# Performance work log

Measured on AMD Instinct MI355X. Metric: run time of the kernel, lower is better.

## Reference

```python
import jax, jax.numpy as jnp
import numpy as np

# ---- static config (matches init_kwargs) ----
D = 1152      # hidden_size
I = 4608      # mlp intermediate = 4*D
DEPTH = 2     # transformer blocks
SA_DEPTH = 3  # spatial adapter depth
P_LAT = 2     # latent patch size
OUT_C = 8     # in_channels*2 (learn_sigma)
FREQ = 256    # timestep frequency embedding size
NV = 4        # num_views
B = 2         # true batch (BN = B*NV = 8)
LAT = 32      # latent H=W
COND = 512    # conditioning image H=W

# ---- BitNet b1.58 / HGRN primitives ----

def rmsnorm(x, eps=1e-8):
    return x * jax.lax.rsqrt(jnp.mean(jnp.square(x), axis=-1, keepdims=True) + eps)

def layernorm(x, gamma=None, beta=None, eps=1e-6):
    mu = jnp.mean(x, axis=-1, keepdims=True)
    xc = x - mu
    y = xc * jax.lax.rsqrt(jnp.mean(jnp.square(xc), axis=-1, keepdims=True) + eps)
    if gamma is not None:
        y = y * gamma + beta
    return y

def _act_quant(x):  # per-token int8 absmax quantization
    s = 127.0 / jnp.clip(jnp.max(jnp.abs(x), axis=-1, keepdims=True), 1e-5, None)
    return jnp.clip(jnp.round(x * s), -128.0, 127.0) / s

def _w_quant(w):    # ternary (1.58-bit) weight quantization, global absmean scale
    s = 1.0 / jnp.clip(jnp.mean(jnp.abs(w)), 1e-5, None)
    return jnp.clip(jnp.round(w * s), -1.0, 1.0) / s

def _ste(x, q):     # straight-through estimator
    return x + jax.lax.stop_gradient(q - x)

def bitlinear(x, w, b=None):
    # FusedBitLinear: RMSNorm -> int8 act quant -> ternary weight matmul
    xn = rmsnorm(x)
    y = _ste(xn, _act_quant(xn)) @ _ste(w, _w_quant(w)).T
    return y if b is None else y + b

def conv2d(x, w, b, stride):
    y = jax.lax.conv_general_dilated(x, w, (stride, stride), 'VALID',
                                     dimension_numbers=('NCHW', 'OIHW', 'NCHW'))
    return y + b[None, :, None, None]

def hgrn_attn(x, wi, wf, wg, wo):
    # HGRN gated-linear attention: h_t = f_t*h_{t-1} + silu(i_t)*(1-f_t),
    # output RMSNorm-swish-gated then o-projected. Element-wise recurrence.
    f = jax.nn.sigmoid(bitlinear(x, wf))
    v = jax.nn.silu(bitlinear(x, wi)) * (1.0 - f)
    g = bitlinear(x, wg)
    def step(h, fv):
        ft, vt = fv
        h = ft * h + vt
        return h, h
    _, o = jax.lax.scan(step, jnp.zeros_like(v[:, 0]),
                        (jnp.swapaxes(f, 0, 1), jnp.swapaxes(v, 0, 1)))
    o = jnp.swapaxes(o, 0, 1)
    o = rmsnorm(o) * g * jax.nn.sigmoid(g)
    return bitlinear(o, wo)

def hgrn_mlp(x, w_gate, w_down):
    gate, y = jnp.split(bitlinear(x, w_gate), 2, axis=-1)
    return bitlinear(jax.nn.silu(gate) * y, w_down)

def modulate(x, shift, scale):
    return x * (1.0 + scale[:, None]) + shift[:, None]

# ---- full adapter forward ----

def _forward(x, t, y, x_cond, ref_tokens, num_views, P):
    BN = x.shape[0]
    # conditioning vector c = TimestepEmbedder(t) + prompt_proj(y)
    half = FREQ // 2
    freqs = jnp.exp(-np.log(10000.0) * jnp.arange(half, dtype=jnp.float32) / half)
    ang = t[:, None] * freqs[None]
    t_emb = jnp.concatenate([jnp.cos(ang), jnp.sin(ang)], axis=-1)
    t_emb = bitlinear(jax.nn.silu(bitlinear(t_emb, P['te_w1'], P['te_b1'])), P['te_w2'], P['te_b2'])
    c = t_emb + bitlinear(y, P['pp_w'], P['pp_b'])

    h = conv2d(x_cond, P['sa_pe_w'], P['sa_pe_b'], 16)      # [BN, D, 32, 32]
    Hc = h.shape[-1]
    h = h.reshape(BN, D, Hc * Hc).transpose(0, 2, 1)
    feats = []
    for i in range(SA_DEPTH):
        h = hgrn_mlp(layernorm(h, P['sa_ln_g'][i], P['sa_ln_b'][i], eps=1e-5),
                     P['sa_gate_w'][i], P['sa_down_w'][i])
        h = h.transpose(0, 2, 1).reshape(BN, D, Hc, Hc)
        h = conv2d(h, P['sa_dc_w'][i], P['sa_dc_b'][i], 2)
        Hc //= 2
        h = h.reshape(BN, D, Hc * Hc).transpose(0, 2, 1)
        feats.append(h)

    # patchify latents + pos embed + spatial cond feature (grid-matched)
    xt = conv2d(x, P['xe_w'], P['xe_b'], P_LAT)             # [BN, D, 16, 16]
    Hp = xt.shape[-1]
    xt = xt.reshape(BN, D, Hp * Hp).transpose(0, 2, 1) + P['pos_embed'] + feats[0]
    L = xt.shape[1]
    b = BN // num_views
    ref_rep = jnp.repeat(ref_tokens, num_views, axis=0)     # repeat_interleave dim 0

    for l in range(DEPTH):
        mod = bitlinear(jax.nn.silu(c), P['blk_ada_w'][l], P['blk_ada_b'][l])
        sh_a, sc_a, g_a, sh_m, sc_m, g_m = jnp.split(mod, 6, axis=-1)
        xm = modulate(layernorm(xt), sh_a, sc_a)
        self_out = hgrn_attn(xm, P['blk_sa_wi'][l], P['blk_sa_wf'][l], P['blk_sa_wg'][l], P['blk_sa_wo'][l])
        # multi-view attention: sequence axis = views
        mv_in = xm.reshape(b, num_views, L, D).transpose(0, 2, 1, 3).reshape(b * L, num_views, D)
        mv_out = hgrn_attn(mv_in, P['blk_mv_wi'][l], P['blk_mv_wf'][l], P['blk_mv_wg'][l], P['blk_mv_wo'][l])
        mv_out = mv_out.reshape(b, L, num_views, D).transpose(0, 2, 1, 3).reshape(BN, L, D)
        ref_out = hgrn_attn(ref_rep, P['blk_rf_wi'][l], P['blk_rf_wf'][l], P['blk_rf_wg'][l], P['blk_rf_wo'][l])
        xt = xt + g_a[:, None] * (self_out + mv_out + ref_out)
        xm = modulate(layernorm(xt), sh_m, sc_m)
        xt = xt + g_m[:, None] * hgrn_mlp(xm, P['blk_gate_w'][l], P['blk_down_w'][l])

    # final layer + unpatchify
    mod = bitlinear(jax.nn.silu(c), P['fl_ada_w'], P['fl_ada_b'])
    shift, scale = jnp.split(mod, 2, axis=-1)
    xt = bitlinear(modulate(layernorm(xt), shift, scale), P['fl_w'], P['fl_b'])
    xt = xt.reshape(BN, Hp, Hp, P_LAT, P_LAT, OUT_C).transpose(0, 5, 1, 3, 2, 4)
    return xt.reshape(BN, OUT_C, Hp * P_LAT, Hp * P_LAT)

PARAM_SHAPES = {
    'xe_w': (D, 4, P_LAT, P_LAT), 'xe_b': (D,), 'pos_embed': (1, 256, D),
    'te_w1': (D, FREQ), 'te_b1': (D,), 'te_w2': (D, D), 'te_b2': (D,),
    'pp_w': (D, 768), 'pp_b': (D,),
    'sa_pe_w': (D, 6, 16, 16), 'sa_pe_b': (D,),
    'sa_ln_g': (SA_DEPTH, D), 'sa_ln_b': (SA_DEPTH, D),
    'sa_gate_w': (SA_DEPTH, 2 * I, D), 'sa_down_w': (SA_DEPTH, D, I),
    'sa_dc_w': (SA_DEPTH, D, D, 2, 2), 'sa_dc_b': (SA_DEPTH, D),
    'blk_ada_w': (DEPTH, 6 * D, D), 'blk_ada_b': (DEPTH, 6 * D),
    'blk_sa_wi': (DEPTH, D, D), 'blk_sa_wf': (DEPTH, D, D), 'blk_sa_wg': (DEPTH, D, D), 'blk_sa_wo': (DEPTH, D, D),
    'blk_mv_wi': (DEPTH, D, D), 'blk_mv_wf': (DEPTH, D, D), 'blk_mv_wg': (DEPTH, D, D), 'blk_mv_wo': (DEPTH, D, D),
    'blk_rf_wi': (DEPTH, D, D), 'blk_rf_wf': (DEPTH, D, D), 'blk_rf_wg': (DEPTH, D, D), 'blk_rf_wo': (DEPTH, D, D),
    'blk_gate_w': (DEPTH, 2 * I, D), 'blk_down_w': (DEPTH, D, I),
    'fl_w': (P_LAT * P_LAT * OUT_C, D), 'fl_b': (P_LAT * P_LAT * OUT_C,),
    'fl_ada_w': (2 * D, D), 'fl_ada_b': (2 * D,),
}
_ZEROS = {'xe_b', 'te_b1', 'te_b2', 'pp_b', 'sa_pe_b', 'sa_ln_b', 'sa_dc_b',
          'blk_ada_b', 'fl_b', 'fl_ada_b'}
_ONES = {'sa_ln_g'}

def setup_inputs() -> dict:
    key = jax.random.key(0)
    ks = iter(jax.random.split(key, 8 + len(PARAM_SHAPES)))
    inp = {
        'x': jax.random.normal(next(ks), (B * NV, 4, LAT, LAT), jnp.float32),
        't': jax.random.uniform(next(ks), (B * NV,), jnp.float32, 0.0, 1000.0),
        'y': jax.random.normal(next(ks), (B * NV, 768), jnp.float32),
        'x_cond': jax.random.normal(next(ks), (B * NV, 6, COND, COND), jnp.float32),
        'ref_tokens': jax.random.normal(next(ks), (B, 256, D), jnp.float32),
        'num_views': NV,
    }
    for name, shp in PARAM_SHAPES.items():
        if name in _ZEROS:
            inp[name] = jnp.zeros(shp, jnp.float32)
        elif name in _ONES:
            inp[name] = jnp.ones(shp, jnp.float32)
        else:
            inp[name] = 0.02 * jax.random.normal(next(ks), shp, jnp.float32)
    return inp

def reference(x, t, y, x_cond, ref_tokens, num_views,
              xe_w, xe_b, pos_embed, te_w1, te_b1, te_w2, te_b2, pp_w, pp_b,
              sa_pe_w, sa_pe_b, sa_ln_g, sa_ln_b, sa_gate_w, sa_down_w, sa_dc_w, sa_dc_b,
              blk_ada_w, blk_ada_b,
              blk_sa_wi, blk_sa_wf, blk_sa_wg, blk_sa_wo,
              blk_mv_wi, blk_mv_wf, blk_mv_wg, blk_mv_wo,
              blk_rf_wi, blk_rf_wf, blk_rf_wg, blk_rf_wo,
              blk_gate_w, blk_down_w, fl_w, fl_b, fl_ada_w, fl_ada_b):
    P = dict(xe_w=xe_w, xe_b=xe_b, pos_embed=pos_embed, te_w1=te_w1, te_b1=te_b1,
             te_w2=te_w2, te_b2=te_b2, pp_w=pp_w, pp_b=pp_b, sa_pe_w=sa_pe_w,
             sa_pe_b=sa_pe_b, sa_ln_g=sa_ln_g, sa_ln_b=sa_ln_b, sa_gate_w=sa_gate_w,
             sa_down_w=sa_down_w, sa_dc_w=sa_dc_w, sa_dc_b=sa_dc_b, blk_ada_w=blk_ada_w,
             blk_ada_b=blk_ada_b, blk_sa_wi=blk_sa_wi, blk_sa_wf=blk_sa_wf,
             blk_sa_wg=blk_sa_wg, blk_sa_wo=blk_sa_wo, blk_mv_wi=blk_mv_wi,
             blk_mv_wf=blk_mv_wf, blk_mv_wg=blk_mv_wg, blk_mv_wo=blk_mv_wo,
             blk_rf_wi=blk_rf_wi, blk_rf_wf=blk_rf_wf, blk_rf_wg=blk_rf_wg,
             blk_rf_wo=blk_rf_wo, blk_gate_w=blk_gate_w, blk_down_w=blk_down_w,
             fl_w=fl_w, fl_b=fl_b, fl_ada_w=fl_ada_w, fl_ada_b=fl_ada_b)
    return _forward(x, t, y, x_cond, ref_tokens, int(num_views), P)
```

## Files before the change

kernel.cpp:

```cpp
#include <hip/hip_runtime.h>

#define DEV __device__ __forceinline__

typedef __attribute__((ext_vector_type(4))) int i32x4;
typedef __attribute__((ext_vector_type(4))) double f64x4;


struct WList { const float* p[37]; long long n[37]; };
struct WOffs { long long o[37]; };

DEV int2 xcd_swz(int gridx)
{
    const int nwg = (int)gridDim.x, b = (int)blockIdx.x;
    const int q = nwg >> 3, r = nwg & 7, xcd = b & 7, idx = b >> 3;
    const int lb = (xcd < r ? xcd*(q+1) : r*(q+1) + (xcd-r)*q) + idx;
    return make_int2(lb % gridx, lb / gridx);
}

__global__ void k_mfma64_probe(double* __restrict__ out)
{
    const int lane = threadIdx.x;
    double a = (double)(1 + lane);
    double b = (double)(101 + 3*lane);
    f64x4 acc = {0.0, 0.0, 0.0, 0.0};
    acc = __builtin_amdgcn_mfma_f64_16x16x4f64(a, b, acc, 0, 0, 0);
#pragma unroll
    for (int r = 0; r < 4; ++r) out[lane*4 + r] = acc[r];
}

__global__ void k_mfma64_check(const double* __restrict__ probe, int* __restrict__ flag)
{
    if (threadIdx.x != 0) return;
    int best = 0;
    for (int c = 0; c < 16 && !best; ++c) {
        const int a_alt = c & 1, b_alt = (c >> 1) & 1, dv = (c >> 2) & 3;
        double Amat[16][4], Bmat[4][16];
        for (int l = 0; l < 64; ++l) {
            int ai = a_alt ? (l >> 2) : (l & 15);
            int ak = a_alt ? (l & 3)  : (l >> 4);
            Amat[ai][ak] = (double)(1 + l);
            int bj = b_alt ? (l >> 2) : (l & 15);
            int bk = b_alt ? (l & 3)  : (l >> 4);
            Bmat[bk][bj] = (double)(101 + 3*l);
        }
        double C[16][16];
        for (int i = 0; i < 16; ++i)
            for (int j = 0; j < 16; ++j) {
                double s = 0.0;
                for (int k = 0; k < 4; ++k) s += Amat[i][k] * Bmat[k][j];
                C[i][j] = s;
            }
        bool ok = true;
        for (int l = 0; l < 64 && ok; ++l)
            for (int r = 0; r < 4 && ok; ++r) {
                int ir = (dv & 2) ? (4*r + (l >> 4)) : (4*(l >> 4) + r);
                int ic = l & 15;
                if (dv & 1) { int t = ir; ir = ic; ic = t; }
                if (probe[l*4 + r] != C[ir][ic]) ok = false;
            }
        if (ok) best = 1 + c;
    }
    *flag = best;
}

__global__ void k_abssum_all(WList wl, double* __restrict__ partials)
{
    const int slot = blockIdx.y;
    const float* w = wl.p[slot];
    const long long n = wl.n[slot];
    __shared__ double sm[256];
    double s = 0.0;
    for (long long i = (long long)blockIdx.x*256 + threadIdx.x; i < n; i += 32LL*256)
        s += (double)fabsf(w[i]);
    sm[threadIdx.x] = s;
    __syncthreads();
    for (int k = 128; k > 0; k >>= 1) {
        if ((int)threadIdx.x < k) sm[threadIdx.x] += sm[threadIdx.x + k];
        __syncthreads();
    }
    if (threadIdx.x == 0) partials[slot*32 + blockIdx.x] = sm[0];
}

__global__ void k_abssum_fin(const double* __restrict__ partials, double* __restrict__ out)
{
    const int slot = blockIdx.x;
    if (threadIdx.x == 0) {
        double s = 0.0;
        for (int i = 0; i < 32; ++i) s += partials[slot*32 + i];
        out[slot] = s;
    }
}

__global__ void k_ternarize(WList wl, WOffs wo, const double* __restrict__ scales,
                            signed char* __restrict__ W8)
{
    const int slot = blockIdx.y;
    const float* w = wl.p[slot];
    const long long n4 = wl.n[slot] >> 2;
    const double dqw = fmax(scales[slot] / (double)wl.n[slot], 1e-5);
    const double thr = 0.5 * dqw;
    signed char* o = W8 + wo.o[slot];
    for (long long i = (long long)blockIdx.x*256 + threadIdx.x; i < n4; i += 64LL*256) {
        float4 v = *reinterpret_cast<const float4*>(w + i*4);
        float we[4] = {v.x, v.y, v.z, v.w};
        char r[4];
#pragma unroll
        for (int e = 0; e < 4; ++e) {
            double wd = (double)we[e];
            r[e] = (char)((wd > thr) - (wd < -thr));
        }
        *reinterpret_cast<char4*>(o + i*4) = make_char4(r[0], r[1], r[2], r[3]);
    }
}

__global__ void k_temb(const float* __restrict__ t, double* __restrict__ out)
{
    int b = blockIdx.x, j = threadIdx.x;
    double fr  = exp(-9.210340371976184 * (double)j / 128.0);
    double ang = (double)t[b] * fr;
    out[b*256 + j]       = cos(ang);
    out[b*256 + 128 + j] = sin(ang);
}

template<typename TI>
__global__ void k_rsq8(const TI* __restrict__ x, signed char* __restrict__ q8,
                       double* __restrict__ dscale, int K, int pre_silu)
{
    __shared__ double red[256], red2[256];
    const int row = blockIdx.x, tid = threadIdx.x;
    const TI* xr = x + (size_t)row*K;
    double ss = 0.0, am = 0.0;
    for (int i = tid; i < K; i += 256) {
        double v = (double)xr[i];
        if (pre_silu) v = v / (1.0 + exp(-v));
        ss += v*v; am = fmax(am, fabs(v));
    }
    red[tid] = ss; red2[tid] = am;
    __syncthreads();
    for (int s = 128; s > 0; s >>= 1) {
        if (tid < s) { red[tid] += red[tid+s]; red2[tid] = fmax(red2[tid], red2[tid+s]); }
        __syncthreads();
    }
    double rms = 1.0 / sqrt(red[0]/(double)K + 1e-8);
    double s   = 127.0 / fmax(red2[0]*rms, 1e-5);
    signed char* orow = q8 + (size_t)row*K;
    for (int i = tid; i < K; i += 256) {
        double v = (double)xr[i];
        if (pre_silu) v = v / (1.0 + exp(-v));
        orow[i] = (signed char)(int)fmin(fmax(rint(v*rms*s), -128.0), 127.0);
    }
    if (tid == 0) dscale[row] = s;
}

__global__ void k_lnq8(const double* __restrict__ x, signed char* __restrict__ q8,
                       double* __restrict__ dscale, int K,
                       const float* __restrict__ gamma, const float* __restrict__ beta,
                       const double* __restrict__ sh, const double* __restrict__ sc,
                       int modstride, double eps)
{
    extern __shared__ double rb[];
    __shared__ double red[256], red2[256];
    const int row = blockIdx.x, tid = threadIdx.x;
    const double* xr = x + (size_t)row*K;
    double s1 = 0.0;
    for (int i = tid; i < K; i += 256) { double v = xr[i]; rb[i] = v; s1 += v; }
    red[tid] = s1; __syncthreads();
    for (int s = 128; s > 0; s >>= 1) { if (tid < s) red[tid] += red[tid+s]; __syncthreads(); }
    double mu = red[0]/(double)K;
    __syncthreads();
    double s2 = 0.0;
    for (int i = tid; i < K; i += 256) { double d = rb[i]-mu; s2 += d*d; }
    red[tid] = s2; __syncthreads();
    for (int s = 128; s > 0; s >>= 1) { if (tid < s) red[tid] += red[tid+s]; __syncthreads(); }
    double r = 1.0 / sqrt(red[0]/(double)K + eps);
    const int bn = row >> 8;
    __syncthreads();
    double ss = 0.0, am = 0.0;
    for (int i = tid; i < K; i += 256) {
        double y = (rb[i]-mu)*r;
        if (gamma) y = y*(double)gamma[i] + (double)beta[i];
        if (sh)    y = y*(1.0 + sc[(size_t)bn*modstride + i]) + sh[(size_t)bn*modstride + i];
        rb[i] = y; ss += y*y; am = fmax(am, fabs(y));
    }
    red[tid] = ss; red2[tid] = am;
    __syncthreads();
    for (int s = 128; s > 0; s >>= 1) {
        if (tid < s) { red[tid] += red[tid+s]; red2[tid] = fmax(red2[tid], red2[tid+s]); }
        __syncthreads();
    }
    double rms = 1.0 / sqrt(red[0]/(double)K + 1e-8);
    double s   = 127.0 / fmax(red2[0]*rms, 1e-5);
    signed char* orow = q8 + (size_t)row*K;
    for (int i = tid; i < K; i += 256)
        orow[i] = (signed char)(int)fmin(fmax(rint(rb[i]*rms*s), -128.0), 127.0);
    if (tid == 0) dscale[row] = s;
}

__global__ void k_ogateq8(const double* __restrict__ O, const double* __restrict__ G,
                          signed char* __restrict__ q8, double* __restrict__ dscale, int K)
{
    extern __shared__ double rb[];
    __shared__ double red[256], red2[256];
    const int row = blockIdx.x, tid = threadIdx.x;
    const double* orow = O + (size_t)row*K;
    const double* grow = G + (size_t)row*K;
    double ss = 0.0;
    for (int i = tid; i < K; i += 256) { double v = orow[i]; rb[i] = v; ss += v*v; }
    red[tid] = ss; __syncthreads();
    for (int s = 128; s > 0; s >>= 1) { if (tid < s) red[tid] += red[tid+s]; __syncthreads(); }
    double rmso = 1.0 / sqrt(red[0]/(double)K + 1e-8);
    __syncthreads();
    double ss2 = 0.0, am = 0.0;
    for (int i = tid; i < K; i += 256) {
        double g = grow[i];
        double y = rb[i]*rmso * g / (1.0 + exp(-g));
        rb[i] = y; ss2 += y*y; am = fmax(am, fabs(y));
    }
    red[tid] = ss2; red2[tid] = am;
    __syncthreads();
    for (int s = 128; s > 0; s >>= 1) {
        if (tid < s) { red[tid] += red[tid+s]; red2[tid] = fmax(red2[tid], red2[tid+s]); }
        __syncthreads();
    }
    double rms = 1.0 / sqrt(red[0]/(double)K + 1e-8);
    double s   = 127.0 / fmax(red2[0]*rms, 1e-5);
    signed char* qrow = q8 + (size_t)row*K;
    for (int i = tid; i < K; i += 256)
        qrow[i] = (signed char)(int)fmin(fmax(rint(rb[i]*rms*s), -128.0), 127.0);
    if (tid == 0) dscale[row] = s;
}

__global__ void k_gatepre(double* __restrict__ F, double* __restrict__ I, long long n)
{
    long long i = (long long)blockIdx.x*256 + threadIdx.x;
    if (i >= n) return;
    double fp = F[i], ip = I[i];
    double f = 1.0/(1.0+exp(-fp));
    double v = (ip/(1.0+exp(-ip)))*(1.0-f);
    F[i] = f; I[i] = v;
}

__global__ void k_scan2(const double* __restrict__ F, const double* __restrict__ V,
                        double* __restrict__ O, int n_outer, long long outer_stride,
                        int n_inner, long long t_stride, int T)
{
    long long chain = (long long)blockIdx.x*blockDim.x + threadIdx.x;
    if (chain >= (long long)n_outer*n_inner) return;
    long long base = (chain / n_inner)*outer_stride + (chain % n_inner);
    double h = 0.0;
    for (int t = 0; t < T; ++t) {
        long long idx = base + (long long)t*t_stride;
        h = F[idx]*h + V[idx];
        O[idx] = h;
    }
}

__global__ void k_add(const double* __restrict__ a, const double* __restrict__ b,
                      double* __restrict__ o, int n)
{
    int i = blockIdx.x*256 + threadIdx.x;
    if (i < n) o[i] = a[i] + b[i];
}

__global__ void k_resid_attn(double* __restrict__ xt, const double* __restrict__ acc,
                             const double* __restrict__ refo, const double* __restrict__ mod)
{
    int idx = blockIdx.x*256 + threadIdx.x;
    int r = idx / 1152, d = idx - r*1152;
    int bn = r >> 8, l = r & 255;
    double ga = mod[(size_t)bn*6912 + 2*1152 + d];
    double rv = refo[((size_t)((bn>>2)*256 + l))*1152 + d];
    xt[idx] += ga*(acc[idx] + rv);
}

__global__ void k_resid_mlp(double* __restrict__ xt, const double* __restrict__ t2,
                            const double* __restrict__ mod)
{
    int idx = blockIdx.x*256 + threadIdx.x;
    int r = idx / 1152, d = idx - r*1152;
    int bn = r >> 8;
    xt[idx] += mod[(size_t)bn*6912 + 5*1152 + d] * t2[idx];
}

__global__ void k_patchify(const float* __restrict__ x, const float* __restrict__ w,
                           const float* __restrict__ bias, const float* __restrict__ pos,
                           const double* __restrict__ f0, double* __restrict__ xt)
{
    int idx = blockIdx.x*256 + threadIdx.x;
    int r = idx / 1152, o = idx - r*1152;
    int bn = r >> 8, p = r & 255;
    int y = p >> 4, xx = p & 15;
    double acc = (double)bias[o] + (double)pos[(size_t)p*1152 + o] + f0[idx];
#pragma unroll
    for (int c = 0; c < 4; ++c)
#pragma unroll
        for (int ky = 0; ky < 2; ++ky)
#pragma unroll
            for (int kx = 0; kx < 2; ++kx)
                acc += (double)x[((size_t)(bn*4 + c)*32 + 2*y+ky)*32 + 2*xx+kx]
                     * (double)w[o*16 + c*4 + ky*2 + kx];
    xt[idx] = acc;
}

__global__ void k_unpatch(const double* __restrict__ flo, float* __restrict__ out)
{
    int idx = blockIdx.x*256 + threadIdx.x;
    int xx = idx & 31, y = (idx>>5)&31, ch = (idx>>10)&7, b = idx>>13;
    int hp = y>>1, py = y&1, wp = xx>>1, px = xx&1;
    out[idx] = (float)flo[((size_t)(b*256 + hp*16 + wp))*32 + (py*2+px)*8 + ch];
}

template<int AMODE>
DEV void load_a4d(const void* __restrict__ A, int row, int k, int M, double o[4])
{
    if (row >= M) { o[0]=o[1]=o[2]=o[3]=0.0; return; }
    if constexpr (AMODE == 1) {
        const float* Af = (const float*)A;
        int b = row>>10, p = row&1023, oy = p>>5, ox = p&31;
        int c = k>>8, ky = (k>>4)&15, kx = k&15;
        float4 v = *reinterpret_cast<const float4*>(
            Af + (((size_t)(b*6+c)*512 + (size_t)(oy*16+ky))*512 + (size_t)(ox*16+kx)));
        o[0]=v.x; o[1]=v.y; o[2]=v.z; o[3]=v.w;
    } else {
        const double* Ad = (const double*)A;
        int b = row>>8, y = (row>>4)&15, x = row&15;
        int q = k/1152, c = k - q*1152, ky = q>>1, kx = q&1;
        const double* p = Ad + (size_t)(b*1024 + (2*y+ky)*32 + 2*x+kx)*1152 + c;
        o[0]=p[0]; o[1]=p[1]; o[2]=p[2]; o[3]=p[3];
    }
}

template<int WMODE>
DEV void load_w4d(const float* __restrict__ W, int row, int k, int Nb, int K, double o[4])
{
    if (row >= Nb) { o[0]=o[1]=o[2]=o[3]=0.0; return; }
    if constexpr (WMODE == 0) {
        float4 v = *reinterpret_cast<const float4*>(W + (size_t)row*K + k);
        o[0]=v.x; o[1]=v.y; o[2]=v.z; o[3]=v.w;
    } else {
        int q = k/1152, c = k - q*1152;
        const float* p = W + (size_t)row*4608 + (size_t)c*4 + q;
        o[0]=p[0]; o[1]=p[4]; o[2]=p[8]; o[3]=p[12];
    }
}

template<int AMODE, int WMODE>
__global__ __launch_bounds__(256)
void k_dgemm(const void* __restrict__ A, const float* __restrict__ W,
             const float* __restrict__ bias, double* __restrict__ C,
             int M, int N, int K, int gridx, const int* __restrict__ mfma_flag)
{
    __shared__ double As[64][17];
    __shared__ double Ws[64][17];
    const int tid = threadIdx.x;
    const int2 bxy = xcd_swz(gridx);
    const int m0 = bxy.y*64, n0 = bxy.x*64;
    const int lr = tid >> 2;
    const int lc = (tid & 3) * 4;
    const int flag = *mfma_flag;

    if (flag) {
        const int cmb = flag - 1;
        const int a_alt = cmb & 1, b_alt = (cmb >> 1) & 1, dv = (cmb >> 2) & 3;
        const int lane = tid & 63, wid = tid >> 6;
        const int wm = wid >> 1, wn = wid & 1;
        const int ai = a_alt ? (lane >> 2) : (lane & 15);
        const int ak = a_alt ? (lane & 3)  : (lane >> 4);
        const int bj = b_alt ? (lane >> 2) : (lane & 15);
        const int bk = b_alt ? (lane & 3)  : (lane >> 4);
        f64x4 fa[2][2];
#pragma unroll
        for (int i = 0; i < 2; ++i)
#pragma unroll
            for (int j = 0; j < 2; ++j) fa[i][j] = f64x4{0.0,0.0,0.0,0.0};

        for (int kt = 0; kt < K; kt += 16) {
            {
                double v[4];
                load_a4d<AMODE>(A, m0+lr, kt+lc, M, v);
                As[lr][lc+0]=v[0]; As[lr][lc+1]=v[1]; As[lr][lc+2]=v[2]; As[lr][lc+3]=v[3];
            }
            {
                double wv[4];
                load_w4d<WMODE>(W, n0+lr, kt+lc, N, K, wv);
                Ws[lr][lc+0]=wv[0]; Ws[lr][lc+1]=wv[1]; Ws[lr][lc+2]=wv[2]; Ws[lr][lc+3]=wv[3];
            }
            __syncthreads();
#pragma unroll
            for (int k4 = 0; k4 < 4; ++k4) {
                double a0 = As[wm*32 + ai][k4*4 + ak];
                double a1 = As[wm*32 + 16 + ai][k4*4 + ak];
                double b0 = Ws[wn*32 + bj][k4*4 + bk];
                double b1 = Ws[wn*32 + 16 + bj][k4*4 + bk];
                fa[0][0] = __builtin_amdgcn_mfma_f64_16x16x4f64(a0, b0, fa[0][0], 0, 0, 0);
                fa[0][1] = __builtin_amdgcn_mfma_f64_16x16x4f64(a0, b1, fa[0][1], 0, 0, 0);
                fa[1][0] = __builtin_amdgcn_mfma_f64_16x16x4f64(a1, b0, fa[1][0], 0, 0, 0);
                fa[1][1] = __builtin_amdgcn_mfma_f64_16x16x4f64(a1, b1, fa[1][1], 0, 0, 0);
            }
            __syncthreads();
        }
#pragma unroll
        for (int i = 0; i < 2; ++i)
#pragma unroll
            for (int j = 0; j < 2; ++j)
#pragma unroll
                for (int r = 0; r < 4; ++r) {
                    int ir = (dv & 2) ? (4*r + (lane >> 4)) : (4*(lane >> 4) + r);
                    int ic = lane & 15;
                    if (dv & 1) { int t = ir; ir = ic; ic = t; }
                    int row = m0 + wm*32 + i*16 + ir;
                    int col = n0 + wn*32 + j*16 + ic;
                    if (row < M && col < N)
                        C[(size_t)row*N + col] = fa[i][j][r] + (bias ? (double)bias[col] : 0.0);
                }
        return;
    }

    const int tx = tid & 15, ty = tid >> 4;
    double acc[4][4] = {};
    for (int kt = 0; kt < K; kt += 16) {
        {
            double v[4];
            load_a4d<AMODE>(A, m0+lr, kt+lc, M, v);
            As[lr][lc+0]=v[0]; As[lr][lc+1]=v[1]; As[lr][lc+2]=v[2]; As[lr][lc+3]=v[3];
        }
        {
            double wv[4];
            load_w4d<WMODE>(W, n0+lr, kt+lc, N, K, wv);
            Ws[lr][lc+0]=wv[0]; Ws[lr][lc+1]=wv[1]; Ws[lr][lc+2]=wv[2]; Ws[lr][lc+3]=wv[3];
        }
        __syncthreads();
#pragma unroll
        for (int k = 0; k < 16; ++k) {
            double a[4], b[4];
#pragma unroll
            for (int e = 0; e < 4; ++e) { a[e] = As[ty + 16*e][k]; b[e] = Ws[tx + 16*e][k]; }
#pragma unroll
            for (int i = 0; i < 4; ++i)
#pragma unroll
                for (int j = 0; j < 4; ++j) acc[i][j] += a[i]*b[j];
        }
        __syncthreads();
    }
#pragma unroll
    for (int i = 0; i < 4; ++i) {
        int row = m0 + ty + 16*i;
        if (row >= M) continue;
#pragma unroll
        for (int j = 0; j < 4; ++j) {
            int col = n0 + tx + 16*j;
            if (col >= N) continue;
            C[(size_t)row*N + col] = acc[i][j] + (bias ? (double)bias[col] : 0.0);
        }
    }
}

template<int GATE, int PRE>
__global__ __launch_bounds__(256)
void k_qgemm(const signed char* __restrict__ A8, const double* __restrict__ ascale,
             const float* __restrict__ Wf, const signed char* __restrict__ W8,
             const double* __restrict__ wsum, long long wcount,
             const float* __restrict__ bias, double* __restrict__ C,
             int M, int N, int K, int accum, int gridM)
{
    __shared__ __align__(16) signed char Als[4][128][16];
    __shared__ __align__(16) signed char Bls[4][128][16];
    __shared__ __align__(16) signed char B2ls[GATE?4:1][GATE?128:1][16];
    const int tid = threadIdx.x;
    const int lane = tid & 63, wid = tid >> 6;
    const int wr = wid >> 1, wc = wid & 1;
    const int2 bxy = xcd_swz(gridM);
    const int m0 = bxy.x*128, n0 = bxy.y*128;
    const int ks = lane >> 4, fr = lane & 15;

    const double dqw = fmax(*wsum / (double)wcount, 1e-5);
    const double thr = 0.5 * dqw;

    i32x4 acc[4][4];
    i32x4 acc2[GATE?4:1][4];
#pragma unroll
    for (int i = 0; i < 4; ++i)
#pragma unroll
        for (int j = 0; j < 4; ++j) {
            acc[i][j] = i32x4{0,0,0,0};
            if constexpr (GATE) acc2[i][j] = i32x4{0,0,0,0};
        }

    for (int kt = 0; kt < K; kt += 64) {
#pragma unroll
        for (int c = 0; c < 2; ++c) {
            int idx = tid + c*256;
            int row = idx & 127, kslot = idx >> 7;
            i32x4 v = {0,0,0,0};
            if (m0 + row < M)
                v = *reinterpret_cast<const i32x4*>(A8 + (size_t)(m0+row)*K + kt + kslot*16);
            *reinterpret_cast<i32x4*>(&Als[kslot][row][0]) = v;
        }
#pragma unroll
        for (int c = 0; c < 2; ++c) {
            int idx = tid + c*256;
            int row = idx & 127, kslot = idx >> 7;
            i32x4 pv = {0,0,0,0};
            if (n0 + row < N) {
                if constexpr (PRE) {
                    pv = *reinterpret_cast<const i32x4*>(W8 + (size_t)(n0+row)*K + kt + kslot*16);
                } else {
                    const float* wp = Wf + (size_t)(n0+row)*K + kt + kslot*16;
#pragma unroll
                    for (int d = 0; d < 4; ++d) {
                        float4 wv = *reinterpret_cast<const float4*>(wp + d*4);
                        float we[4] = {wv.x, wv.y, wv.z, wv.w};
                        unsigned p = 0;
#pragma unroll
                        for (int e = 0; e < 4; ++e) {
                            double wd = (double)we[e];
                            int q = (wd > thr) - (wd < -thr);
                            p |= ((unsigned)(q & 255)) << (8*e);
                        }
                        pv[d] = (int)p;
                    }
                }
            }
            *reinterpret_cast<i32x4*>(&Bls[kslot][row][0]) = pv;
        }
        if constexpr (GATE) {
#pragma unroll
            for (int c = 0; c < 2; ++c) {
                int idx = tid + c*256;
                int row = idx & 127, kslot = idx >> 7;
                i32x4 pv = {0,0,0,0};
                if (n0 + row < N) {
                    if constexpr (PRE) {
                        pv = *reinterpret_cast<const i32x4*>(W8 + (size_t)(n0+row+N)*K + kt + kslot*16);
                    } else {
                        const float* wp = Wf + (size_t)(n0+row+N)*K + kt + kslot*16;
#pragma unroll
                        for (int d = 0; d < 4; ++d) {
                            float4 wv = *reinterpret_cast<const float4*>(wp + d*4);
                            float we[4] = {wv.x, wv.y, wv.z, wv.w};
                            unsigned p = 0;
#pragma unroll
                            for (int e = 0; e < 4; ++e) {
                                double wd = (double)we[e];
                                int q = (wd > thr) - (wd < -thr);
                                p |= ((unsigned)(q & 255)) << (8*e);
                            }
                            pv[d] = (int)p;
                        }
                    }
                }
                *reinterpret_cast<i32x4*>(&B2ls[kslot][row][0]) = pv;
            }
        }
        __syncthreads();
        i32x4 a[4];
#pragma unroll
        for (int i = 0; i < 4; ++i)
            a[i] = *reinterpret_cast<const i32x4*>(&Als[ks][wr*64 + i*16 + fr][0]);
#pragma unroll
        for (int j = 0; j < 4; ++j) {
            i32x4 b = *reinterpret_cast<const i32x4*>(&Bls[ks][wc*64 + j*16 + fr][0]);
#pragma unroll
            for (int i = 0; i < 4; ++i)
                acc[i][j] = __builtin_amdgcn_mfma_i32_16x16x64_i8(a[i], b, acc[i][j], 0, 0, 0);
            if constexpr (GATE) {
                i32x4 b2 = *reinterpret_cast<const i32x4*>(&B2ls[ks][wc*64 + j*16 + fr][0]);
#pragma unroll
                for (int i = 0; i < 4; ++i)
                    acc2[i][j] = __builtin_amdgcn_mfma_i32_16x16x64_i8(a[i], b2, acc2[i][j], 0, 0, 0);
            }
        }
        __syncthreads();
    }

#pragma unroll
    for (int i = 0; i < 4; ++i) {
#pragma unroll
        for (int r = 0; r < 4; ++r) {
            int row = m0 + wr*64 + i*16 + (lane>>4)*4 + r;
            if (row >= M) continue;
            double mul = dqw / ascale[row];
#pragma unroll
            for (int j = 0; j < 4; ++j) {
                int col = n0 + wc*64 + j*16 + (lane & 15);
                if (col >= N) continue;
                size_t o = (size_t)row*N + col;
                if constexpr (GATE) {
                    double g = (double)acc[i][j][r] * mul;
                    double y = (double)acc2[i][j][r] * mul;
                    C[o] = g/(1.0+exp(-g)) * y;
                } else {
                    double v = (double)acc[i][j][r] * mul;
                    if (bias) v += (double)bias[col];
                    C[o] = accum ? C[o] + v : v;
                }
            }
        }
    }
}

extern "C" void kernel_launch(void* const* d_in, const int* in_sizes, int n_in,
                              void* d_out, int out_size, void* d_ws, size_t ws_size,
                              hipStream_t stream)
{
    (void)in_sizes; (void)n_in; (void)out_size;
    auto in = [&](int i){ return (const float*)d_in[i]; };

    const float *X = in(0), *T = in(1), *Y = in(2), *XC = in(3), *REF = in(4);
    const float *xe_w = in(6), *xe_b = in(7), *pos = in(8);
    const float *te_w1 = in(9), *te_b1 = in(10), *te_w2 = in(11), *te_b2 = in(12);
    const float *pp_w = in(13), *pp_b = in(14);
    const float *sa_pe_w = in(15), *sa_pe_b = in(16);
    const float *sa_ln_g = in(17), *sa_ln_b = in(18);
    const float *sa_gate_w = in(19), *sa_down_w = in(20);
    const float *sa_dc_w = in(21), *sa_dc_b = in(22);
    const float *ada_w = in(23), *ada_b = in(24);
    const float *sa_wi = in(25), *sa_wf = in(26), *sa_wg = in(27), *sa_wo = in(28);
    const float *mv_wi = in(29), *mv_wf = in(30), *mv_wg = in(31), *mv_wo = in(32);
    const float *rf_wi = in(33), *rf_wf = in(34), *rf_wg = in(35), *rf_wo = in(36);
    const float *gate_w = in(37), *down_w = in(38);
    const float *fl_w = in(39), *fl_b = in(40), *fl_ada_w = in(41), *fl_ada_b = in(42);
    float* OUT = (float*)d_out;

    size_t off = 0;
    auto AL = [&](size_t bytes){ off = (off+255)&~(size_t)255; size_t r = off; off += bytes; return r; };
    const size_t oScale = AL(37*8);
    const size_t oPart  = AL(37*32*8);
    const size_t oProbe = AL(64*4*8);
    const size_t oFlag  = AL(256);
    const size_t oSM1 = AL(8*1152*8), oSM2 = AL(8*1152*8), oSM3 = AL(8*1152*8);
    const size_t oCB  = AL(8*1152*8);
    const size_t oMOD = AL(8*6912*8);
    const size_t oH   = AL((size_t)8192*1152*8);
    const size_t oINT = AL((size_t)1024*4608*8);
    const size_t oF0  = AL((size_t)2048*1152*8);
    const size_t oXT  = AL((size_t)2048*1152*8);
    const size_t oFB  = AL((size_t)2048*1152*8);
    const size_t oIB  = AL((size_t)2048*1152*8);
    const size_t oGB  = AL((size_t)2048*1152*8);
    const size_t oRO  = AL((size_t)512*1152*8);
    const size_t oQ8X = AL((size_t)2048*1152);
    const size_t oQ8I = AL((size_t)1024*4608);
    const size_t oQ8O = AL((size_t)2048*1152);
    const size_t oQ8R = AL((size_t)512*1152);
    const size_t oQ8T = AL((size_t)8*1152);
    const size_t oQ8C = AL((size_t)8*1152);
    const size_t oDSX = AL(2048*8), oDSI = AL(1024*8), oDSO = AL(2048*8);
    const size_t oDSR = AL(512*8),  oDST = AL(8*8),    oDSC = AL(8*8);
    if (off > ws_size) return;

    WList wl{}; WOffs wo{};
    long long wn[37];
    int nw = 0;
    auto addw = [&](const float* w, long long n){ wl.p[nw]=w; wl.n[nw]=n; wn[nw]=n; nw++; };
    addw(te_w1, 294912); addw(te_w2, 1327104); addw(pp_w, 884736);
    addw(sa_gate_w, 10616832); addw(sa_down_w, 5308416);
    for (int l = 0; l < 2; ++l) {
        addw(ada_w + (size_t)l*7962624, 7962624);
        addw(sa_wi + (size_t)l*1327104, 1327104);
        addw(sa_wf + (size_t)l*1327104, 1327104);
        addw(sa_wg + (size_t)l*1327104, 1327104);
        addw(sa_wo + (size_t)l*1327104, 1327104);
        addw(mv_wi + (size_t)l*1327104, 1327104);
        addw(mv_wf + (size_t)l*1327104, 1327104);
        addw(mv_wg + (size_t)l*1327104, 1327104);
        addw(mv_wo + (size_t)l*1327104, 1327104);
        addw(rf_wi + (size_t)l*1327104, 1327104);
        addw(rf_wf + (size_t)l*1327104, 1327104);
        addw(rf_wg + (size_t)l*1327104, 1327104);
        addw(rf_wo + (size_t)l*1327104, 1327104);
        addw(gate_w + (size_t)l*10616832, 10616832);
        addw(down_w + (size_t)l*5308416, 5308416);
    }
    addw(fl_ada_w, 2654208); addw(fl_w, 36864);

    size_t off_saved = off;
    long long wtot = 0;
    for (int i = 0; i < 37; ++i) { wo.o[i] = wtot; wtot += (wn[i] + 255) & ~255LL; }
    const size_t oW8 = AL((size_t)wtot);
    const bool useW8 = (off <= ws_size);
    if (!useW8) off = off_saved;

    int schunk = 1024;
    size_t oINTb = 0, oQ8Ib = 0, oQ8Xb = 0, oDSXb = 0, oDSIb = 0;
    if (useW8) {
        size_t off_w8 = off;
        oINTb = AL((size_t)4096*4608*8); oQ8Ib = AL((size_t)4096*4608);
        oQ8Xb = AL((size_t)4096*1152);   oDSXb = AL(4096*8); oDSIb = AL(4096*8);
        if (off <= ws_size) schunk = 4096;
        else {
            off = off_w8;
            oINTb = AL((size_t)2048*4608*8); oQ8Ib = AL((size_t)2048*4608); oDSIb = AL(2048*8);
            if (off <= ws_size) schunk = 2048;
            else off = off_w8;
        }
    }

    char* w8p = (char*)d_ws;
    double* scales = (double*)(w8p + oScale);
    double* parts  = (double*)(w8p + oPart);
    double* probeD = (double*)(w8p + oProbe);
    int*    mflag  = (int*)(w8p + oFlag);
    double *SM1=(double*)(w8p+oSM1), *SM2=(double*)(w8p+oSM2), *SM3=(double*)(w8p+oSM3);
    double *CB=(double*)(w8p+oCB), *MOD=(double*)(w8p+oMOD);
    double *H=(double*)(w8p+oH), *INT=(double*)(w8p+oINT);
    double *F0=(double*)(w8p+oF0), *XT=(double*)(w8p+oXT);
    double *FB=(double*)(w8p+oFB), *IB=(double*)(w8p+oIB), *GB=(double*)(w8p+oGB);
    double *ACC=F0, *OB=H, *RO=(double*)(w8p+oRO);
    signed char *Q8X=(signed char*)(w8p+oQ8X), *Q8I=(signed char*)(w8p+oQ8I);
    signed char *Q8O=(signed char*)(w8p+oQ8O), *Q8R=(signed char*)(w8p+oQ8R);
    signed char *Q8T=(signed char*)(w8p+oQ8T), *Q8C=(signed char*)(w8p+oQ8C);
    double *DSX=(double*)(w8p+oDSX), *DSI=(double*)(w8p+oDSI), *DSO=(double*)(w8p+oDSO);
    double *DSR=(double*)(w8p+oDSR), *DST=(double*)(w8p+oDST), *DSC=(double*)(w8p+oDSC);
    signed char* W8 = (signed char*)(w8p + oW8);

    double*      INTs = (schunk > 1024) ? (double*)(w8p + oINTb) : INT;
    signed char* Q8Is = (schunk > 1024) ? (signed char*)(w8p + oQ8Ib) : Q8I;
    double*      DSIs = (schunk > 1024) ? (double*)(w8p + oDSIb) : DSI;
    signed char* Q8Xs = (schunk == 4096) ? (signed char*)(w8p + oQ8Xb) : Q8X;
    double*      DSXs = (schunk == 4096) ? (double*)(w8p + oDSXb) : DSX;

    k_mfma64_probe<<<1, 64, 0, stream>>>(probeD);
    k_mfma64_check<<<1, 64, 0, stream>>>(probeD, mflag);
    k_abssum_all<<<dim3(32,37), 256, 0, stream>>>(wl, parts);
    k_abssum_fin<<<37, 64, 0, stream>>>(parts, scales);
    if (useW8)
        k_ternarize<<<dim3(64,37), 256, 0, stream>>>(wl, wo, scales, W8);

    auto qgemm = [&](const signed char* A8, const double* as, const float* Win, int slot,
                     const float* b, double* Cout, int M, int N, int K, int accum){
        int gm = (M+127)/128, gn = (N+127)/128;
        if (useW8)
            k_qgemm<0,1><<<gm*gn, 256, 0, stream>>>(A8, as, Win, W8 + wo.o[slot],
                                                    scales+slot, wn[slot], b, Cout, M, N, K, accum, gm);
        else
            k_qgemm<0,0><<<gm*gn, 256, 0, stream>>>(A8, as, Win, nullptr,
                                                    scales+slot, wn[slot], b, Cout, M, N, K, accum, gm);
    };
    auto qgemmGate = [&](const signed char* A8, const double* as, const float* Win, int slot,
                         double* Cout, int M){
        int gm = (M+127)/128;
        if (useW8)
            k_qgemm<1,1><<<gm*36, 256, 0, stream>>>(A8, as, Win, W8 + wo.o[slot],
                                                    scales+slot, wn[slot], nullptr, Cout, M, 4608, 1152, 0, gm);
        else
            k_qgemm<1,0><<<gm*36, 256, 0, stream>>>(A8, as, Win, nullptr,
                                                    scales+slot, wn[slot], nullptr, Cout, M, 4608, 1152, 0, gm);
    };

    k_temb<<<8, 128, 0, stream>>>(T, SM1);
    k_rsq8<double><<<8, 256, 0, stream>>>(SM1, Q8T, DST, 256, 0);
    qgemm(Q8T, DST, te_w1, 0, te_b1, SM3, 8, 1152, 256, 0);
    k_rsq8<double><<<8, 256, 0, stream>>>(SM3, Q8T, DST, 1152, 1);
    qgemm(Q8T, DST, te_w2, 1, te_b2, SM2, 8, 1152, 1152, 0);
    k_rsq8<float><<<8, 256, 0, stream>>>(Y, Q8T, DST, 768, 0);
    qgemm(Q8T, DST, pp_w, 2, pp_b, SM3, 8, 1152, 768, 0);
    k_add<<<36, 256, 0, stream>>>(SM2, SM3, CB, 9216);
    k_rsq8<double><<<8, 256, 0, stream>>>(CB, Q8C, DSC, 1152, 1);

    k_dgemm<1,0><<<18*128, 256, 0, stream>>>(XC, sa_pe_w, sa_pe_b, H, 8192, 1152, 1536, 18, mflag);
    {
        const int nch = 8192 / schunk;
        for (int ch = 0; ch < nch; ++ch) {
            double* Hrow = H + (size_t)ch*schunk*1152;
            k_lnq8<<<schunk, 256, 1152*8, stream>>>(Hrow, Q8Xs, DSXs, 1152, sa_ln_g, sa_ln_b,
                                                    nullptr, nullptr, 0, 1e-5);
            qgemmGate(Q8Xs, DSXs, sa_gate_w, 3, INTs, schunk);
            k_rsq8<double><<<schunk, 256, 0, stream>>>(INTs, Q8Is, DSIs, 4608, 0);
            qgemm(Q8Is, DSIs, sa_down_w, 4, nullptr, Hrow, schunk, 1152, 4608, 0);
        }
    }
    k_dgemm<2,1><<<18*32, 256, 0, stream>>>(H, sa_dc_w, sa_dc_b, F0, 2048, 1152, 4608, 18, mflag);

    k_patchify<<<9216, 256, 0, stream>>>(X, xe_w, xe_b, pos, F0, XT);
    k_rsq8<float><<<512, 256, 0, stream>>>(REF, Q8R, DSR, 1152, 0);

    for (int l = 0; l < 2; ++l) {
        int sb = 5 + l*15;
        const float *wada = ada_w + (size_t)l*7962624, *bada = ada_b + (size_t)l*6912;
        const float *swi = sa_wi + (size_t)l*1327104, *swf = sa_wf + (size_t)l*1327104;
        const float *swg = sa_wg + (size_t)l*1327104, *swo = sa_wo + (size_t)l*1327104;
        const float *mwi = mv_wi + (size_t)l*1327104, *mwf = mv_wf + (size_t)l*1327104;
        const float *mwg = mv_wg + (size_t)l*1327104, *mwo = mv_wo + (size_t)l*1327104;
        const float *rwi = rf_wi + (size_t)l*1327104, *rwf = rf_wf + (size_t)l*1327104;
        const float *rwg = rf_wg + (size_t)l*1327104, *rwo = rf_wo + (size_t)l*1327104;
        const float *wgt = gate_w + (size_t)l*10616832, *wdn = down_w + (size_t)l*5308416;

        qgemm(Q8C, DSC, wada, sb+0, bada, MOD, 8, 6912, 1152, 0);

        k_lnq8<<<2048, 256, 1152*8, stream>>>(XT, Q8X, DSX, 1152, nullptr, nullptr,
                                              MOD+0, MOD+1152, 6912, 1e-6);

        qgemm(Q8X, DSX, swf, sb+2, nullptr, FB, 2048, 1152, 1152, 0);
        qgemm(Q8X, DSX, swi, sb+1, nullptr, IB, 2048, 1152, 1152, 0);
        qgemm(Q8X, DSX, swg, sb+3, nullptr, GB, 2048, 1152, 1152, 0);
        k_gatepre<<<9216, 256, 0, stream>>>(FB, IB, 2359296LL);
        k_scan2<<<36, 256, 0, stream>>>(FB, IB, OB, 8, 294912LL, 1152, 1152LL, 256);
        k_ogateq8<<<2048, 256, 1152*8, stream>>>(OB, GB, Q8O, DSO, 1152);
        qgemm(Q8O, DSO, swo, sb+4, nullptr, ACC, 2048, 1152, 1152, 0);

        qgemm(Q8X, DSX, mwf, sb+6, nullptr, FB, 2048, 1152, 1152, 0);
        qgemm(Q8X, DSX, mwi, sb+5, nullptr, IB, 2048, 1152, 1152, 0);
        qgemm(Q8X, DSX, mwg, sb+7, nullptr, GB, 2048, 1152, 1152, 0);
        k_gatepre<<<9216, 256, 0, stream>>>(FB, IB, 2359296LL);
        k_scan2<<<2304, 256, 0, stream>>>(FB, IB, OB, 2, 1179648LL, 294912, 294912LL, 4);
        k_ogateq8<<<2048, 256, 1152*8, stream>>>(OB, GB, Q8O, DSO, 1152);
        qgemm(Q8O, DSO, mwo, sb+8, nullptr, ACC, 2048, 1152, 1152, 1);

        qgemm(Q8R, DSR, rwf, sb+10, nullptr, FB, 512, 1152, 1152, 0);
        qgemm(Q8R, DSR, rwi, sb+9,  nullptr, IB, 512, 1152, 1152, 0);
        qgemm(Q8R, DSR, rwg, sb+11, nullptr, GB, 512, 1152, 1152, 0);
        k_gatepre<<<2304, 256, 0, stream>>>(FB, IB, 589824LL);
        k_scan2<<<9, 256, 0, stream>>>(FB, IB, OB, 2, 294912LL, 1152, 1152LL, 256);
        k_ogateq8<<<512, 256, 1152*8, stream>>>(OB, GB, Q8O, DSO, 1152);
        qgemm(Q8O, DSO, rwo, sb+12, nullptr, RO, 512, 1152, 1152, 0);

        k_resid_attn<<<9216, 256, 0, stream>>>(XT, ACC, RO, MOD);

        k_lnq8<<<2048, 256, 1152*8, stream>>>(XT, Q8X, DSX, 1152, nullptr, nullptr,
                                              MOD+3*1152, MOD+4*1152, 6912, 1e-6);
        if (schunk >= 2048) {
            qgemmGate(Q8X, DSX, wgt, sb+13, INTs, 2048);
            k_rsq8<double><<<2048, 256, 0, stream>>>(INTs, Q8Is, DSIs, 4608, 0);
            qgemm(Q8Is, DSIs, wdn, sb+14, nullptr, OB, 2048, 1152, 4608, 0);
        } else {
            for (int ch = 0; ch < 2; ++ch) {
                qgemmGate(Q8X + (size_t)ch*1024*1152, DSX + ch*1024, wgt, sb+13, INT, 1024);
                k_rsq8<double><<<1024, 256, 0, stream>>>(INT, Q8I, DSI, 4608, 0);
                qgemm(Q8I, DSI, wdn, sb+14, nullptr, OB + (size_t)ch*1024*1152, 1024, 1152, 4608, 0);
            }
        }
        k_resid_mlp<<<9216, 256, 0, stream>>>(XT, OB, MOD);
    }

    qgemm(Q8C, DSC, fl_ada_w, 35, fl_ada_b, MOD, 8, 2304, 1152, 0);
    k_lnq8<<<2048, 256, 1152*8, stream>>>(XT, Q8X, DSX, 1152, nullptr, nullptr,
                                          MOD+0, MOD+1152, 2304, 1e-6);
    qgemm(Q8X, DSX, fl_w, 36, fl_b, FB, 2048, 32, 1152, 0);
    k_unpatch<<<256, 256, 0, stream>>>(FB, OUT);
}
```

Measured before the change: 5.163 ms.

## Fuse F/I/G projections into one GEMM launch and pre-transpose conv weight

Introduces k_qgemm3, which computes the forget, input and gate projections for HGRN in a single launch, applying sigmoid and silu in its epilogue. A new scan kernel folds the (1-f) multiply in, so the separate gatepre pass and two extra GEMM launches are removed. The spatial-adapter deconv weight is also pre-transposed into workspace once so the dgemm can read it contiguously. This trades extra workspace use and a per-call transpose for fewer launches and fewer memory passes.

```diff
diff --git a/kernel.cpp b/kernel.cpp
--- a/kernel.cpp
+++ b/kernel.cpp
@@ -8,6 +8,7 @@
 
 struct WList { const float* p[37]; long long n[37]; };
 struct WOffs { long long o[37]; };
+struct W3 { const signed char* w[3]; const double* sc[3]; double* c[3]; };
 
 DEV int2 xcd_swz(int gridx)
 {
@@ -110,6 +111,15 @@
             r[e] = (char)((wd > thr) - (wd < -thr));
         }
         *reinterpret_cast<char4*>(o + i*4) = make_char4(r[0], r[1], r[2], r[3]);
+    }
+}
+
+__global__ void k_dcw_prep(const float* __restrict__ w, float* __restrict__ wt)
+{
+    int row = blockIdx.x;
+    for (int k = threadIdx.x; k < 4608; k += 256) {
+        int q = k / 1152, c = k - q*1152;
+        wt[(size_t)row*4608 + k] = w[(size_t)row*4608 + (size_t)c*4 + q];
     }
 }
 
@@ -255,6 +265,23 @@
     }
 }
 
+__global__ void k_scan3(const double* __restrict__ F, const double* __restrict__ Isilu,
+                        double* __restrict__ O, int n_outer, long long outer_stride,
+                        int n_inner, long long t_stride, int T)
+{
+    long long chain = (long long)blockIdx.x*blockDim.x + threadIdx.x;
+    if (chain >= (long long)n_outer*n_inner) return;
+    long long base = (chain / n_inner)*outer_stride + (chain % n_inner);
+    double h = 0.0;
+    for (int t = 0; t < T; ++t) {
+        long long idx = base + (long long)t*t_stride;
+        double f = F[idx];
+        double v = Isilu[idx]*(1.0-f);
+        h = f*h + v;
+        O[idx] = h;
+    }
+}
+
 __global__ void k_add(const double* __restrict__ a, const double* __restrict__ b,
                       double* __restrict__ o, int n)
 {
@@ -594,6 +621,83 @@
                     if (bias) v += (double)bias[col];
                     C[o] = accum ? C[o] + v : v;
                 }
+            }
+        }
+    }
+}
+
+__global__ __launch_bounds__(256)
+void k_qgemm3(const signed char* __restrict__ A8, const double* __restrict__ ascale,
+              W3 w3, long long wcount, int M, int gridM)
+{
+    __shared__ __align__(16) signed char Als[4][128][16];
+    __shared__ __align__(16) signed char Bls[4][128][16];
+    const int tid = threadIdx.x;
+    const int lane = tid & 63, wid = tid >> 6;
+    const int wr = wid >> 1, wc = wid & 1;
+    const int2 bxy = xcd_swz(gridM);
+    const int m0 = bxy.x*128;
+    const int yy = bxy.y;
+    const int g = yy / 9, nt = yy - g*9;
+    const int n0 = nt*128;
+    const signed char* W8 = w3.w[g];
+    double* C = w3.c[g];
+    const int ks = lane >> 4, fr = lane & 15;
+
+    const double dqw = fmax(*w3.sc[g] / (double)wcount, 1e-5);
+
+    i32x4 acc[4][4];
+#pragma unroll
+    for (int i = 0; i < 4; ++i)
+#pragma unroll
+        for (int j = 0; j < 4; ++j) acc[i][j] = i32x4{0,0,0,0};
+
+    for (int kt = 0; kt < 1152; kt += 64) {
+#pragma unroll
+        for (int c = 0; c < 2; ++c) {
+            int idx = tid + c*256;
+            int row = idx & 127, kslot = idx >> 7;
+            i32x4 v = {0,0,0,0};
+            if (m0 + row < M)
+                v = *reinterpret_cast<const i32x4*>(A8 + (size_t)(m0+row)*1152 + kt + kslot*16);
+            *reinterpret_cast<i32x4*>(&Als[kslot][row][0]) = v;
+        }
+#pragma unroll
+        for (int c = 0; c < 2; ++c) {
+            int idx = tid + c*256;
+            int row = idx & 127, kslot = idx >> 7;
+            i32x4 pv = *reinterpret_cast<const i32x4*>(W8 + (size_t)(n0+row)*1152 + kt + kslot*16);
+            *reinterpret_cast<i32x4*>(&Bls[kslot][row][0]) = pv;
+        }
+        __syncthreads();
+        i32x4 a[4];
+#pragma unroll
+        for (int i = 0; i < 4; ++i)
+            a[i] = *reinterpret_cast<const i32x4*>(&Als[ks][wr*64 + i*16 + fr][0]);
+#pragma unroll
+        for (int j = 0; j < 4; ++j) {
+            i32x4 b = *reinterpret_cast<const i32x4*>(&Bls[ks][wc*64 + j*16 + fr][0]);
+#pragma unroll
+            for (int i = 0; i < 4; ++i)
+                acc[i][j] = __builtin_amdgcn_mfma_i32_16x16x64_i8(a[i], b, acc[i][j], 0, 0, 0);
+        }
+        __syncthreads();
+    }
+
+#pragma unroll
+    for (int i = 0; i < 4; ++i) {
+#pragma unroll
+        for (int r = 0; r < 4; ++r) {
+            int row = m0 + wr*64 + i*16 + (lane>>4)*4 + r;
+            if (row >= M) continue;
+            double mul = dqw / ascale[row];
+#pragma unroll
+            for (int j = 0; j < 4; ++j) {
+                int col = n0 + wc*64 + j*16 + (lane & 15);
+                double v = (double)acc[i][j][r] * mul;
+                if (g == 0)      v = 1.0/(1.0+exp(-v));
+                else if (g == 1) v = v/(1.0+exp(-v));
+                C[(size_t)row*1152 + col] = v;
             }
         }
     }
@@ -681,6 +785,11 @@
     const bool useW8 = (off <= ws_size);
     if (!useW8) off = off_saved;
 
+    size_t off_wt = off;
+    const size_t oWt = AL((size_t)1152*4608*4);
+    const bool useWt = (off <= ws_size);
+    if (!useWt) off = off_wt;
+
     int schunk = 1024;
     size_t oINTb = 0, oQ8Ib = 0, oQ8Xb = 0, oDSXb = 0, oDSIb = 0;
     if (useW8) {
@@ -713,6 +822,7 @@
     double *DSX=(double*)(w8p+oDSX), *DSI=(double*)(w8p+oDSI), *DSO=(double*)(w8p+oDSO);
     double *DSR=(double*)(w8p+oDSR), *DST=(double*)(w8p+oDST), *DSC=(double*)(w8p+oDSC);
     signed char* W8 = (signed char*)(w8p + oW8);
+    float* Wt = (float*)(w8p + oWt);
 
     double*      INTs = (schunk > 1024) ? (double*)(w8p + oINTb) : INT;
     signed char* Q8Is = (schunk > 1024) ? (signed char*)(w8p + oQ8Ib) : Q8I;
@@ -726,6 +836,8 @@
     k_abssum_fin<<<37, 64, 0, stream>>>(parts, scales);
     if (useW8)
         k_ternarize<<<dim3(64,37), 256, 0, stream>>>(wl, wo, scales, W8);
+    if (useWt)
+        k_dcw_prep<<<1152, 256, 0, stream>>>(sa_dc_w, Wt);
 
     auto qgemm = [&](const signed char* A8, const double* as, const float* Win, int slot,
                      const float* b, double* Cout, int M, int N, int K, int accum){
@@ -747,6 +859,27 @@
             k_qgemm<1,0><<<gm*36, 256, 0, stream>>>(A8, as, Win, nullptr,
                                                     scales+slot, wn[slot], nullptr, Cout, M, 4608, 1152, 0, gm);
     };
+    auto fig = [&](const signed char* A8, const double* as, int sF, int sI, int sG,
+                   const float* wF, const float* wI, const float* wG, int M,
+                   int n_outer, long long ostr, int n_inner, long long tstr, int Tlen){
+        if (useW8) {
+            W3 w3{ {W8+wo.o[sF], W8+wo.o[sI], W8+wo.o[sG]},
+                   {scales+sF, scales+sI, scales+sG},
+                   {FB, IB, GB} };
+            int gm = M/128;
+            k_qgemm3<<<gm*27, 256, 0, stream>>>(A8, as, w3, 1327104, M, gm);
+            long long nch = (long long)n_outer*n_inner;
+            k_scan3<<<(unsigned)((nch+255)/256), 256, 0, stream>>>(FB, IB, OB, n_outer, ostr, n_inner, tstr, Tlen);
+        } else {
+            qgemm(A8, as, wF, sF, nullptr, FB, M, 1152, 1152, 0);
+            qgemm(A8, as, wI, sI, nullptr, IB, M, 1152, 1152, 0);
+            qgemm(A8, as, wG, sG, nullptr, GB, M, 1152, 1152, 0);
+            long long nel = (long long)M*1152;
+            k_gatepre<<<(unsigned)((nel+255)/256), 256, 0, stream>>>(FB, IB, nel);
+            long long nch = (long long)n_outer*n_inner;
+            k_scan2<<<(unsigned)((nch+255)/256), 256, 0, stream>>>(FB, IB, OB, n_outer, ostr, n_inner, tstr, Tlen);
+        }
+    };
 
     k_temb<<<8, 128, 0, stream>>>(T, SM1);
     k_rsq8<double><<<8, 256, 0, stream>>>(SM1, Q8T, DST, 256, 0);
@@ -770,7 +903,10 @@
             qgemm(Q8Is, DSIs, sa_down_w, 4, nullptr, Hrow, schunk, 1152, 4608, 0);
         }
     }
-    k_dgemm<2,1><<<18*32, 256, 0, stream>>>(H, sa_dc_w, sa_dc_b, F0, 2048, 1152, 4608, 18, mflag);
+    if (useWt)
+        k_dgemm<2,0><<<18*32, 256, 0, stream>>>(H, Wt, sa_dc_b, F0, 2048, 1152, 4608, 18, mflag);
+    else
+        k_dgemm<2,1><<<18*32, 256, 0, stream>>>(H, sa_dc_w, sa_dc_b, F0, 2048, 1152, 4608, 18, mflag);
 
     k_patchify<<<9216, 256, 0, stream>>>(X, xe_w, xe_b, pos, F0, XT);
     k_rsq8<float><<<512, 256, 0, stream>>>(REF, Q8R, DSR, 1152, 0);
@@ -791,27 +927,15 @@
         k_lnq8<<<2048, 256, 1152*8, stream>>>(XT, Q8X, DSX, 1152, nullptr, nullptr,
                                               MOD+0, MOD+1152, 6912, 1e-6);
 
-        qgemm(Q8X, DSX, swf, sb+2, nullptr, FB, 2048, 1152, 1152, 0);
-        qgemm(Q8X, DSX, swi, sb+1, nullptr, IB, 2048, 1152, 1152, 0);
-        qgemm(Q8X, DSX, swg, sb+3, nullptr, GB, 2048, 1152, 1152, 0);
-        k_gatepre<<<9216, 256, 0, stream>>>(FB, IB, 2359296LL);
-        k_scan2<<<36, 256, 0, stream>>>(FB, IB, OB, 8, 294912LL, 1152, 1152LL, 256);
+        fig(Q8X, DSX, sb+2, sb+1, sb+3, swf, swi, swg, 2048, 8, 294912LL, 1152, 1152LL, 256);
         k_ogateq8<<<2048, 256, 1152*8, stream>>>(OB, GB, Q8O, DSO, 1152);
         qgemm(Q8O, DSO, swo, sb+4, nullptr, ACC, 2048, 1152, 1152, 0);
 
-        qgemm(Q8X, DSX, mwf, sb+6, nullptr, FB, 2048, 1152, 1152, 0);
-        qgemm(Q8X, DSX, mwi, sb+5, nullptr, IB, 2048, 1152, 1152, 0);
-        qgemm(Q8X, DSX, mwg, sb+7, nullptr, GB, 2048, 1152, 1152, 0);
-        k_gatepre<<<9216, 256, 0, stream>>>(FB, IB, 2359296LL);
-        k_scan2<<<2304, 256, 0, stream>>>(FB, IB, OB, 2, 1179648LL, 294912, 294912LL, 4);
+        fig(Q8X, DSX, sb+6, sb+5, sb+7, mwf, mwi, mwg, 2048, 2, 1179648LL, 294912, 294912LL, 4);
         k_ogateq8<<<2048, 256, 1152*8, stream>>>(OB, GB, Q8O, DSO, 1152);
         qgemm(Q8O, DSO, mwo, sb+8, nullptr, ACC, 2048, 1152, 1152, 1);
 
-        qgemm(Q8R, DSR, rwf, sb+10, nullptr, FB, 512, 1152, 1152, 0);
-        qgemm(Q8R, DSR, rwi, sb+9,  nullptr, IB, 512, 1152, 1152, 0);
-        qgemm(Q8R, DSR, rwg, sb+11, nullptr, GB, 512, 1152, 1152, 0);
-        k_gatepre<<<2304, 256, 0, stream>>>(FB, IB, 589824LL);
-        k_scan2<<<9, 256, 0, stream>>>(FB, IB, OB, 2, 294912LL, 1152, 1152LL, 256);
+        fig(Q8R, DSR, sb+10, sb+9, sb+11, rwf, rwi, rwg, 512, 2, 294912LL, 1152, 1152LL, 256);
         k_ogateq8<<<512, 256, 1152*8, stream>>>(OB, GB, Q8O, DSO, 1152);
         qgemm(Q8O, DSO, rwo, sb+12, nullptr, RO, 512, 1152, 1152, 0);
 
```

New measurement: 4.849 ms. 6.1% less time.
